# Performance work log

Hardware: AMD Instinct MI355X
Metric: run time of the kernel (lower is better)

Reference implementation:

```python
import jax, jax.numpy as jnp
import numpy as np

N, E, H, IN = 4096, 65536, 256, 16
N_BLOCKS, N_SUB = 3, 2
IE = 2 * H + 2  # edge-mlp input: h[row] ++ h[col] ++ edge_attr(2)
NORM_FACTOR = 100.0


def setup_inputs() -> dict:
    key = jax.random.key(0)
    ks = jax.random.split(key, 24)
    G = N_BLOCKS * N_SUB  # 6 GCLs total

    def p(k, shape, fan_in, gain=1.0):
        return gain * jax.random.normal(k, shape, jnp.float32) / np.sqrt(fan_in)

    return {
        "h": jax.random.normal(ks[0], (N, IN), jnp.float32),
        "x": jax.random.normal(ks[1], (N, 3), jnp.float32),
        "edge_index": jax.random.randint(ks[2], (2, E), 0, N),
        # embedding in/out
        "emb_w": p(ks[3], (IN, H), IN), "emb_b": jnp.zeros((H,), jnp.float32),
        "out_w": p(ks[4], (H, IN), H), "out_b": jnp.zeros((IN,), jnp.float32),
        # GCL edge MLP (stacked over the 6 GCLs)
        "edge_w1": p(ks[5], (G, IE, H), IE), "edge_b1": jnp.zeros((G, H), jnp.float32),
        "edge_w2": p(ks[6], (G, H, H), H), "edge_b2": jnp.zeros((G, H), jnp.float32),
        # GCL node MLP
        "node_w1": p(ks[7], (G, 2 * H, H), 2 * H), "node_b1": jnp.zeros((G, H), jnp.float32),
        "node_w2": p(ks[8], (G, H, H), H), "node_b2": jnp.zeros((G, H), jnp.float32),
        # EquivariantUpdate coord MLP (stacked over 3 blocks); last layer xavier gain=0.001, no bias
        "coord_w1": p(ks[9], (N_BLOCKS, IE, H), IE), "coord_b1": jnp.zeros((N_BLOCKS, H), jnp.float32),
        "coord_w2": p(ks[10], (N_BLOCKS, H, H), H), "coord_b2": jnp.zeros((N_BLOCKS, H), jnp.float32),
        "coord_w3": p(ks[11], (N_BLOCKS, H, 1), H, gain=0.001),
    }


def reference(h, x, edge_index, emb_w, emb_b, out_w, out_b,
              edge_w1, edge_b1, edge_w2, edge_b2,
              node_w1, node_b1, node_w2, node_b2,
              coord_w1, coord_b1, coord_w2, coord_b2, coord_w3):
    row, col = edge_index[0], edge_index[1]
    n_nodes = h.shape[0]

    def seg_sum(data):  # unsorted_segment_sum with 'sum' aggregation / normalization_factor
        return jax.ops.segment_sum(data, row, num_segments=n_nodes) / NORM_FACTOR

    def coord2diff(xc):  # norm_constant = 1
        d = xc[row] - xc[col]                      # [E,3]
        radial = jnp.sum(d * d, axis=1, keepdims=True)  # [E,1]
        cd = d / (jnp.sqrt(radial + 1e-8) + 1.0)
        return radial, cd

    dist0, _ = coord2diff(x)          # EGNN-level distances (from initial coords)
    h = h @ emb_w + emb_b             # node embedding

    gi = 0
    for b in range(N_BLOCKS):
        radial, coord_diff = coord2diff(x)
        ea = jnp.concatenate([radial, dist0], axis=1)   # [E,2] edge_attr
        for _ in range(N_SUB):  # GCL sublayers
            m = jnp.concatenate([h[row], h[col], ea], axis=1)           # [E, 2H+2]
            m = jax.nn.silu(m @ edge_w1[gi] + edge_b1[gi])
            m = jax.nn.silu(m @ edge_w2[gi] + edge_b2[gi])              # [E, H]
            agg = seg_sum(m)                                            # [N, H]
            u = jnp.concatenate([h, agg], axis=1)                       # [N, 2H]
            u = jax.nn.silu(u @ node_w1[gi] + node_b1[gi])
            h = h + u @ node_w2[gi] + node_b2[gi]                       # residual node update
            gi += 1
        # EquivariantUpdate (tanh=False)
        t = jnp.concatenate([h[row], h[col], ea], axis=1)
        t = jax.nn.silu(t @ coord_w1[b] + coord_b1[b])
        t = jax.nn.silu(t @ coord_w2[b] + coord_b2[b])
        trans = coord_diff * (t @ coord_w3[b])                          # [E,3]
        x = x + seg_sum(trans)

    h = h @ out_w + out_b
    return h, x
```

## Files before the change

### kernel.cpp

```cpp
#include <hip/hip_runtime.h>
#include <hip/hip_bf16.h>
#include <cstdint>
#include <cstddef>

#define NN 4096
#define NE 65536
#define HD 256

typedef __attribute__((ext_vector_type(4))) float f32x4;
typedef __attribute__((ext_vector_type(8))) __bf16 bf16x8;

static __device__ __forceinline__ float silu_f(float v) {
  return v / (1.f + __expf(-v));
}

struct TJob { const float* src; __bf16* dst; int K; int N; };
struct TJobs { TJob j[39]; };

__global__ __launch_bounds__(256) void k_transpose(TJobs jobs) {
  TJob jb = jobs.j[blockIdx.z];
  int k0 = blockIdx.x << 5, n0 = blockIdx.y << 5;
  if (k0 >= jb.K || n0 >= jb.N) return;
  __shared__ float t[32][33];
  int tx = threadIdx.x & 31, ty = threadIdx.x >> 5;
#pragma unroll
  for (int r = ty; r < 32; r += 8)
    t[r][tx] = jb.src[(size_t)(k0 + r) * jb.N + n0 + tx];
  __syncthreads();
#pragma unroll
  for (int r = ty; r < 32; r += 8)
    jb.dst[(size_t)(n0 + r) * jb.K + k0 + tx] = (__bf16)t[tx][r];
}

__global__ __launch_bounds__(256) void k_hist(const int* __restrict__ ei, int* __restrict__ cnt) {
  int e = blockIdx.x * 256 + threadIdx.x;
  atomicAdd(&cnt[ei[e]], 1);
}

__global__ __launch_bounds__(1024) void k_scan(const int* __restrict__ cnt, int* __restrict__ offs,
                                               int* __restrict__ cursor) {
  __shared__ int tmp[1024];
  int tid = threadIdx.x;
  int v[4]; int s = 0;
#pragma unroll
  for (int i = 0; i < 4; i++) { v[i] = cnt[tid * 4 + i]; s += v[i]; }
  tmp[tid] = s;
  __syncthreads();
  for (int o = 1; o < 1024; o <<= 1) {
    int t = (tid >= o) ? tmp[tid - o] : 0;
    __syncthreads();
    tmp[tid] += t;
    __syncthreads();
  }
  int base = (tid > 0) ? tmp[tid - 1] : 0;
#pragma unroll
  for (int i = 0; i < 4; i++) {
    offs[tid * 4 + i] = base; cursor[tid * 4 + i] = base; base += v[i];
  }
  if (tid == 1023) offs[4096] = base;
}

__global__ __launch_bounds__(256) void k_scatter(const int* __restrict__ ei, int* __restrict__ cursor,
                                                 int* __restrict__ elist) {
  int e = blockIdx.x * 256 + threadIdx.x;
  int pos = atomicAdd(&cursor[ei[e]], 1);
  elist[pos] = e;
}

__global__ __launch_bounds__(256) void k_csrinit(const int* __restrict__ elist, const int* __restrict__ ei,
                                                 const float* __restrict__ x, int* __restrict__ rowp,
                                                 int* __restrict__ colp, float* __restrict__ d0p) {
  int i = blockIdx.x * 256 + threadIdx.x;
  int e = elist[i];
  int r = ei[e], c = ei[NE + e];
  rowp[i] = r; colp[i] = c;
  float dx = x[r * 3 + 0] - x[c * 3 + 0];
  float dy = x[r * 3 + 1] - x[c * 3 + 1];
  float dz = x[r * 3 + 2] - x[c * 3 + 2];
  d0p[i] = dx * dx + dy * dy + dz * dz;
}

__global__ __launch_bounds__(256) void k_geo(const int* __restrict__ rowp, const int* __restrict__ colp,
                                             const float* __restrict__ x, float* __restrict__ radp,
                                             float* __restrict__ cdp) {
  int i = blockIdx.x * 256 + threadIdx.x;
  int r = rowp[i], c = colp[i];
  float dx = x[r * 3 + 0] - x[c * 3 + 0];
  float dy = x[r * 3 + 1] - x[c * 3 + 1];
  float dz = x[r * 3 + 2] - x[c * 3 + 2];
  float rad = dx * dx + dy * dy + dz * dz;
  radp[i] = rad;
  float inv = 1.f / (sqrtf(rad + 1e-8f) + 1.f);
  cdp[i * 3 + 0] = dx * inv; cdp[i * 3 + 1] = dy * inv; cdp[i * 3 + 2] = dz * inv;
}

__global__ __launch_bounds__(256) void k_copyx(const float* __restrict__ x, float* __restrict__ xc) {
  int i = blockIdx.x * 256 + threadIdx.x;
  if (i < NN * 3) xc[i] = x[i];
}

__global__ __launch_bounds__(256) void k_embed(const float* __restrict__ h0, const float* __restrict__ W,
                                               const float* __restrict__ b, float* __restrict__ hf,
                                               __bf16* __restrict__ h16) {
  int n = blockIdx.x, c = threadIdx.x;
  float s = b[c];
#pragma unroll
  for (int i = 0; i < 16; i++) s += h0[n * 16 + i] * W[i * 256 + c];
  hf[(size_t)n * HD + c] = s;
  h16[(size_t)n * HD + c] = (__bf16)s;
}

__global__ __launch_bounds__(256) void k_segsum(const __bf16* __restrict__ m2p, const int* __restrict__ offs,
                                                const __bf16* __restrict__ h16, __bf16* __restrict__ ncat) {
  __shared__ float sd[8][256];
  int n = blockIdx.x, t = threadIdx.x;
  int g = t >> 5, l = t & 31;
  int c0 = l << 3;
  float a[8] = {};
  int ib = offs[n], ie = offs[n + 1];
  for (int i = ib + g; i < ie; i += 8) {
    bf16x8 v = *(const bf16x8*)(m2p + (size_t)i * 256 + c0);
#pragma unroll
    for (int j = 0; j < 8; j++) a[j] += (float)v[j];
  }
#pragma unroll
  for (int j = 0; j < 8; j++) sd[g][c0 + j] = a[j];
  __syncthreads();
  float s = 0.f;
#pragma unroll
  for (int j = 0; j < 8; j++) s += sd[j][t];
  ncat[(size_t)n * 512 + t] = h16[(size_t)n * HD + t];
  ncat[(size_t)n * 512 + 256 + t] = (__bf16)(s * 0.01f);
}

__global__ __launch_bounds__(256) void k_xupd(const float* __restrict__ transp, const int* __restrict__ offs,
                                              float* __restrict__ xc) {
  int n = blockIdx.x * 256 + threadIdx.x;
  if (n >= NN) return;
  float a0 = 0.f, a1 = 0.f, a2 = 0.f;
  int i1 = offs[n + 1];
  for (int i = offs[n]; i < i1; i++) {
    a0 += transp[i * 3 + 0]; a1 += transp[i * 3 + 1]; a2 += transp[i * 3 + 2];
  }
  xc[n * 3 + 0] += a0 * 0.01f;
  xc[n * 3 + 1] += a1 * 0.01f;
  xc[n * 3 + 2] += a2 * 0.01f;
}

__global__ __launch_bounds__(256) void k_outh(const float* __restrict__ hf, const float* __restrict__ W,
                                              const float* __restrict__ b, float* __restrict__ out) {
  int t = blockIdx.x * 256 + threadIdx.x;
  int n = t >> 4, j = t & 15;
  float s = b[j];
  for (int c = 0; c < 256; c++) s += hf[(size_t)n * HD + c] * W[c * 16 + j];
  out[n * 16 + j] = s;
}

__global__ __launch_bounds__(256) void k_outx(const float* __restrict__ xc, float* __restrict__ out) {
  int i = blockIdx.x * 256 + threadIdx.x;
  if (i < NN * 3) out[i] = xc[i];
}

template <int EPI>
__global__ __launch_bounds__(512, 4) void k_edgeblk(
    const __bf16* __restrict__ PQ, const int* __restrict__ rowp, const int* __restrict__ colp,
    const float* __restrict__ radp, const float* __restrict__ d0p,
    const float* __restrict__ w1r, const float* __restrict__ w1d, const float* __restrict__ b1,
    const __bf16* __restrict__ Bt, const float* __restrict__ b2,
    __bf16* __restrict__ m2p,
    const float* __restrict__ w3, const float* __restrict__ cdp, float* __restrict__ transp) {
  __shared__ alignas(16) char smem[81920];
  __bf16* As = (__bf16*)smem;
  __bf16* Bs = (__bf16*)(smem + 65536);
  float (*reds)[4] = (float(*)[4])smem;

  const int tid = threadIdx.x;
  const int lane = tid & 63;
  const int wave = tid >> 6;
  const int wm = wave >> 2, wn = wave & 3;
  const int m0 = blockIdx.x * 128;

  const int bn = tid >> 1;
  const int bg = (tid & 1) * 2;
  const int bswz0 = (bg ^ ((bn >> 1) & 3)) << 3;
  const int bswz1 = ((bg + 1) ^ ((bn >> 1) & 3)) << 3;

  const int ar = tid >> 2;
  const int aq = tid & 3;
  const int er = rowp[m0 + ar], ec = colp[m0 + ar];
  const float rad = radp[m0 + ar], dd0 = d0p[m0 + ar];

  uint4 br0a = *(const uint4*)(Bt + (size_t)bn * 256 + bg * 8);
  uint4 br0b = *(const uint4*)(Bt + (size_t)bn * 256 + bg * 8 + 8);
  uint4 br1a = *(const uint4*)(Bt + (size_t)bn * 256 + 32 + bg * 8);
  uint4 br1b = *(const uint4*)(Bt + (size_t)bn * 256 + 32 + bg * 8 + 8);
  uint4 breg[2][2];
  breg[0][0] = br0a; breg[0][1] = br0b;
  breg[1][0] = br1a; breg[1][1] = br1b;

#pragma unroll
  for (int i = 0; i < 8; i++) {
    int g = aq + 4 * i;
    int k = g * 8;
    bf16x8 pv = *(const bf16x8*)(PQ + (size_t)er * 512 + k);
    bf16x8 qv = *(const bf16x8*)(PQ + (size_t)ec * 512 + 256 + k);
    float4 wr0 = *(const float4*)(w1r + k),     wr1 = *(const float4*)(w1r + k + 4);
    float4 wd0 = *(const float4*)(w1d + k),     wd1 = *(const float4*)(w1d + k + 4);
    float4 bb0 = *(const float4*)(b1 + k),      bb1 = *(const float4*)(b1 + k + 4);
    bf16x8 o;
    const float* wrp0 = &wr0.x; const float* wdp0 = &wd0.x; const float* bbp0 = &bb0.x;
#pragma unroll
    for (int j = 0; j < 4; j++)
      o[j] = (__bf16)silu_f((float)pv[j] + (float)qv[j] + rad * wrp0[j] + dd0 * wdp0[j] + bbp0[j]);
    const float* wrp1 = &wr1.x; const float* wdp1 = &wd1.x; const float* bbp1 = &bb1.x;
#pragma unroll
    for (int j = 0; j < 4; j++)
      o[4 + j] = (__bf16)silu_f((float)pv[4 + j] + (float)qv[4 + j] + rad * wrp1[j] + dd0 * wdp1[j] + bbp1[j]);
    *(bf16x8*)&As[ar * 256 + ((g ^ (ar & 7)) << 3)] = o;
  }

  *(uint4*)&Bs[bn * 32 + bswz0] = breg[0][0];
  *(uint4*)&Bs[bn * 32 + bswz1] = breg[0][1];
  __syncthreads();

  f32x4 acc[4][4] = {};
  const int kg = lane >> 4;
  const int l15 = lane & 15;

#pragma unroll
  for (int t = 0; t < 8; t++) {
    if (t + 2 < 8) {
      breg[t & 1][0] = *(const uint4*)(Bt + (size_t)bn * 256 + (t + 2) * 32 + bg * 8);
      breg[t & 1][1] = *(const uint4*)(Bt + (size_t)bn * 256 + (t + 2) * 32 + bg * 8 + 8);
    }
    bf16x8 bf[4];
#pragma unroll
    for (int fn = 0; fn < 4; fn++) {
      int n = wn * 64 + fn * 16 + l15;
      bf[fn] = *(const bf16x8*)&Bs[n * 32 + ((kg ^ ((n >> 1) & 3)) << 3)];
    }
#pragma unroll
    for (int fm = 0; fm < 4; fm++) {
      int r = wm * 64 + fm * 16 + l15;
      int G = t * 4 + kg;
      bf16x8 af = *(const bf16x8*)&As[r * 256 + ((G ^ (r & 7)) << 3)];
#pragma unroll
      for (int fn = 0; fn < 4; fn++)
        acc[fm][fn] = __builtin_amdgcn_mfma_f32_16x16x32_bf16(af, bf[fn], acc[fm][fn], 0, 0, 0);
    }
    __syncthreads();
    if (t < 7) {
      *(uint4*)&Bs[bn * 32 + bswz0] = breg[(t + 1) & 1][0];
      *(uint4*)&Bs[bn * 32 + bswz1] = breg[(t + 1) & 1][1];
      __syncthreads();
    }
  }

  if (EPI == 0) {
#pragma unroll
    for (int fm = 0; fm < 4; fm++) {
#pragma unroll
      for (int j = 0; j < 4; j++) {
        size_t row = m0 + wm * 64 + fm * 16 + ((lane >> 4) << 2) + j;
#pragma unroll
        for (int fn = 0; fn < 4; fn++) {
          int col = wn * 64 + fn * 16 + l15;
          m2p[row * 256 + col] = (__bf16)silu_f(acc[fm][fn][j] + b2[col]);
        }
      }
    }
  } else {
    float s[4][4];
#pragma unroll
    for (int fm = 0; fm < 4; fm++)
#pragma unroll
      for (int j = 0; j < 4; j++) s[fm][j] = 0.f;
#pragma unroll
    for (int fn = 0; fn < 4; fn++) {
      int col = wn * 64 + fn * 16 + l15;
      float bv = b2[col], wv = w3[col];
#pragma unroll
      for (int fm = 0; fm < 4; fm++)
#pragma unroll
        for (int j = 0; j < 4; j++)
          s[fm][j] += silu_f(acc[fm][fn][j] + bv) * wv;
    }
#pragma unroll
    for (int off = 1; off < 16; off <<= 1)
#pragma unroll
      for (int fm = 0; fm < 4; fm++)
#pragma unroll
        for (int j = 0; j < 4; j++)
          s[fm][j] += __shfl_xor(s[fm][j], off, 64);
    if (l15 == 0) {
#pragma unroll
      for (int fm = 0; fm < 4; fm++)
#pragma unroll
        for (int j = 0; j < 4; j++)
          reds[wm * 64 + fm * 16 + ((lane >> 4) << 2) + j][wn] = s[fm][j];
    }
    __syncthreads();
    if (tid < 128) {
      float sv = reds[tid][0] + reds[tid][1] + reds[tid][2] + reds[tid][3];
      size_t i = (size_t)m0 + tid;
      transp[i * 3 + 0] = cdp[i * 3 + 0] * sv;
      transp[i * 3 + 1] = cdp[i * 3 + 1] * sv;
      transp[i * 3 + 2] = cdp[i * 3 + 2] * sv;
    }
  }
}

template <int EPI>
__global__ __launch_bounds__(256) void k_gemm64(const __bf16* __restrict__ A, const __bf16* __restrict__ Bt,
                                                const float* __restrict__ bias, __bf16* __restrict__ outb,
                                                float* __restrict__ outf, int M, int N, int K) {
  constexpr int BM = 64, BN = 64, BK = 64;
  __shared__ __bf16 As[2][BM * BK];
  __shared__ __bf16 Bs[2][BN * BK];
  const int tid = threadIdx.x;
  const int lane = tid & 63;
  const int wave = tid >> 6;
  const int wm = wave >> 1, wn = wave & 1;
  const size_t m0 = (size_t)blockIdx.x * BM;
  const size_t n0 = (size_t)blockIdx.y * BN;
  const int r0 = tid >> 3, g0 = tid & 7;
  const int gs0 = (g0 ^ (r0 & 7)) << 3;

  f32x4 acc[2][2] = {};
  const int NT = K >> 6;

  {
    uint4 a0 = *(const uint4*)(A + (m0 + r0) * K + g0 * 8);
    uint4 a1 = *(const uint4*)(A + (m0 + r0 + 32) * K + g0 * 8);
    uint4 b0 = *(const uint4*)(Bt + (n0 + r0) * K + g0 * 8);
    uint4 b1 = *(const uint4*)(Bt + (n0 + r0 + 32) * K + g0 * 8);
    *(uint4*)&As[0][r0 * BK + gs0] = a0;
    *(uint4*)&As[0][(r0 + 32) * BK + gs0] = a1;
    *(uint4*)&Bs[0][r0 * BK + gs0] = b0;
    *(uint4*)&Bs[0][(r0 + 32) * BK + gs0] = b1;
  }
  __syncthreads();

  int buf = 0;
  for (int t = 0; t < NT; ++t) {
    const bool has = (t + 1 < NT);
    uint4 a0, a1, b0, b1;
    if (has) {
      int kt = (t + 1) << 6;
      a0 = *(const uint4*)(A + (m0 + r0) * K + kt + g0 * 8);
      a1 = *(const uint4*)(A + (m0 + r0 + 32) * K + kt + g0 * 8);
      b0 = *(const uint4*)(Bt + (n0 + r0) * K + kt + g0 * 8);
      b1 = *(const uint4*)(Bt + (n0 + r0 + 32) * K + kt + g0 * 8);
    }
#pragma unroll
    for (int ks = 0; ks < BK; ks += 32) {
      const int kg = (ks >> 3) + (lane >> 4);
      bf16x8 af[2], bfv[2];
#pragma unroll
      for (int fm = 0; fm < 2; fm++) {
        int r = wm * 32 + fm * 16 + (lane & 15);
        af[fm] = *(const bf16x8*)&As[buf][r * BK + ((kg ^ (r & 7)) << 3)];
      }
#pragma unroll
      for (int fn = 0; fn < 2; fn++) {
        int r = wn * 32 + fn * 16 + (lane & 15);
        bfv[fn] = *(const bf16x8*)&Bs[buf][r * BK + ((kg ^ (r & 7)) << 3)];
      }
#pragma unroll
      for (int fm = 0; fm < 2; fm++)
#pragma unroll
        for (int fn = 0; fn < 2; fn++)
          acc[fm][fn] = __builtin_amdgcn_mfma_f32_16x16x32_bf16(af[fm], bfv[fn], acc[fm][fn], 0, 0, 0);
    }
    if (has) {
      *(uint4*)&As[buf ^ 1][r0 * BK + gs0] = a0;
      *(uint4*)&As[buf ^ 1][(r0 + 32) * BK + gs0] = a1;
      *(uint4*)&Bs[buf ^ 1][r0 * BK + gs0] = b0;
      *(uint4*)&Bs[buf ^ 1][(r0 + 32) * BK + gs0] = b1;
    }
    __syncthreads();
    buf ^= 1;
  }

#pragma unroll
  for (int fm = 0; fm < 2; fm++) {
#pragma unroll
    for (int fn = 0; fn < 2; fn++) {
      const size_t col = n0 + wn * 32 + fn * 16 + (lane & 15);
      float bv = (EPI == 4) ? 0.f : bias[col];
#pragma unroll
      for (int j = 0; j < 4; j++) {
        size_t row = m0 + wm * 32 + fm * 16 + ((lane >> 4) << 2) + j;
        size_t idx = row * (size_t)N + col;
        float v = acc[fm][fn][j] + bv;
        if (EPI == 1) {
          outb[idx] = (__bf16)silu_f(v);
        } else if (EPI == 2) {
          float nh = outf[idx] + v;
          outf[idx] = nh;
          outb[idx] = (__bf16)nh;
        } else {
          outb[idx] = (__bf16)v;
        }
      }
    }
  }
}

extern "C" void kernel_launch(void* const* d_in, const int* in_sizes, int n_in,
                              void* d_out, int out_size, void* d_ws, size_t ws_size,
                              hipStream_t stream) {
  const float* h_in    = (const float*)d_in[0];
  const float* x_in    = (const float*)d_in[1];
  const int*   ei      = (const int*)d_in[2];
  const float* emb_w   = (const float*)d_in[3];
  const float* emb_b   = (const float*)d_in[4];
  const float* out_w   = (const float*)d_in[5];
  const float* out_b   = (const float*)d_in[6];
  const float* edge_w1 = (const float*)d_in[7];
  const float* edge_b1 = (const float*)d_in[8];
  const float* edge_w2 = (const float*)d_in[9];
  const float* edge_b2 = (const float*)d_in[10];
  const float* node_w1 = (const float*)d_in[11];
  const float* node_b1 = (const float*)d_in[12];
  const float* node_w2 = (const float*)d_in[13];
  const float* node_b2 = (const float*)d_in[14];
  const float* coord_w1 = (const float*)d_in[15];
  const float* coord_b1 = (const float*)d_in[16];
  const float* coord_w2 = (const float*)d_in[17];
  const float* coord_b2 = (const float*)d_in[18];
  const float* coord_w3 = (const float*)d_in[19];

  char* p = (char*)d_ws;
  auto alloc = [&](size_t bytes) -> void* {
    void* r = (void*)p;
    p += (bytes + 255) & ~(size_t)255;
    return r;
  };
  __bf16* e1T  = (__bf16*)alloc((size_t)6 * 512 * 256 * 2);
  __bf16* e2T  = (__bf16*)alloc((size_t)6 * 256 * 256 * 2);
  __bf16* n1T  = (__bf16*)alloc((size_t)6 * 256 * 512 * 2);
  __bf16* n2T  = (__bf16*)alloc((size_t)6 * 256 * 256 * 2);
  __bf16* c1T  = (__bf16*)alloc((size_t)3 * 512 * 256 * 2);
  __bf16* c2T  = (__bf16*)alloc((size_t)3 * 256 * 256 * 2);
  __bf16* h16  = (__bf16*)alloc((size_t)NN * HD * 2);
  __bf16* PQ16 = (__bf16*)alloc((size_t)NN * 512 * 2);
  __bf16* m2p  = (__bf16*)alloc((size_t)NE * HD * 2);
  __bf16* ncat = (__bf16*)alloc((size_t)NN * 512 * 2);
  __bf16* u    = (__bf16*)alloc((size_t)NN * HD * 2);
  float* hf    = (float*)alloc((size_t)NN * HD * 4);
  float* xc    = (float*)alloc((size_t)NN * 3 * 4);
  float* d0p   = (float*)alloc((size_t)NE * 4);
  float* radp  = (float*)alloc((size_t)NE * 4);
  float* cdp   = (float*)alloc((size_t)NE * 3 * 4);
  float* transp = (float*)alloc((size_t)NE * 3 * 4);
  int* cnt     = (int*)alloc((size_t)NN * 4);
  int* offs    = (int*)alloc((size_t)(NN + 1) * 4);
  int* cursor  = (int*)alloc((size_t)NN * 4);
  int* elist   = (int*)alloc((size_t)NE * 4);
  int* rowp    = (int*)alloc((size_t)NE * 4);
  int* colp    = (int*)alloc((size_t)NE * 4);

  TJobs jobs;
  int nj = 0;
  for (int gi = 0; gi < 6; gi++) {
    jobs.j[nj++] = { edge_w1 + (size_t)gi * 514 * 256,             e1T + (size_t)gi * 512 * 256,             256, 256 };
    jobs.j[nj++] = { edge_w1 + (size_t)gi * 514 * 256 + 256 * 256, e1T + (size_t)gi * 512 * 256 + 256 * 256, 256, 256 };
    jobs.j[nj++] = { edge_w2 + (size_t)gi * 256 * 256,             e2T + (size_t)gi * 256 * 256,             256, 256 };
    jobs.j[nj++] = { node_w1 + (size_t)gi * 512 * 256,             n1T + (size_t)gi * 256 * 512,             512, 256 };
    jobs.j[nj++] = { node_w2 + (size_t)gi * 256 * 256,             n2T + (size_t)gi * 256 * 256,             256, 256 };
  }
  for (int b = 0; b < 3; b++) {
    jobs.j[nj++] = { coord_w1 + (size_t)b * 514 * 256,             c1T + (size_t)b * 512 * 256,              256, 256 };
    jobs.j[nj++] = { coord_w1 + (size_t)b * 514 * 256 + 256 * 256, c1T + (size_t)b * 512 * 256 + 256 * 256,  256, 256 };
    jobs.j[nj++] = { coord_w2 + (size_t)b * 256 * 256,             c2T + (size_t)b * 256 * 256,              256, 256 };
  }

  hipMemsetAsync(cnt, 0, (size_t)NN * 4, stream);
  k_transpose<<<dim3(16, 8, 39), 256, 0, stream>>>(jobs);
  k_hist<<<NE / 256, 256, 0, stream>>>(ei, cnt);
  k_scan<<<1, 1024, 0, stream>>>(cnt, offs, cursor);
  k_scatter<<<NE / 256, 256, 0, stream>>>(ei, cursor, elist);
  k_csrinit<<<NE / 256, 256, 0, stream>>>(elist, ei, x_in, rowp, colp, d0p);
  k_copyx<<<(NN * 3 + 255) / 256, 256, 0, stream>>>(x_in, xc);
  k_embed<<<NN, 256, 0, stream>>>(h_in, emb_w, emb_b, hf, h16);

  int gi = 0;
  for (int b = 0; b < 3; b++) {
    k_geo<<<NE / 256, 256, 0, stream>>>(rowp, colp, xc, radp, cdp);
    for (int s = 0; s < 2; s++, gi++) {
      const float* w1 = edge_w1 + (size_t)gi * 514 * 256;
      k_gemm64<4><<<dim3(64, 8), 256, 0, stream>>>(
          h16, e1T + (size_t)gi * 512 * 256, nullptr, PQ16, nullptr, NN, 512, 256);
      k_edgeblk<0><<<NE / 128, 512, 0, stream>>>(
          PQ16, rowp, colp, radp, d0p, w1 + 512 * 256, w1 + 513 * 256, edge_b1 + gi * 256,
          e2T + (size_t)gi * 256 * 256, edge_b2 + gi * 256, m2p, nullptr, nullptr, nullptr);
      k_segsum<<<NN, 256, 0, stream>>>(m2p, offs, h16, ncat);
      k_gemm64<1><<<dim3(64, 4), 256, 0, stream>>>(
          ncat, n1T + (size_t)gi * 256 * 512, node_b1 + gi * 256, u, nullptr, NN, 256, 512);
      k_gemm64<2><<<dim3(64, 4), 256, 0, stream>>>(
          u, n2T + (size_t)gi * 256 * 256, node_b2 + gi * 256, h16, hf, NN, 256, 256);
    }
    const float* w1c = coord_w1 + (size_t)b * 514 * 256;
    k_gemm64<4><<<dim3(64, 8), 256, 0, stream>>>(
        h16, c1T + (size_t)b * 512 * 256, nullptr, PQ16, nullptr, NN, 512, 256);
    k_edgeblk<1><<<NE / 128, 512, 0, stream>>>(
        PQ16, rowp, colp, radp, d0p, w1c + 512 * 256, w1c + 513 * 256, coord_b1 + b * 256,
        c2T + (size_t)b * 256 * 256, coord_b2 + b * 256, nullptr,
        coord_w3 + (size_t)b * 256, cdp, transp);
    k_xupd<<<NN / 256, 256, 0, stream>>>(transp, offs, xc);
  }
  k_outh<<<NN * 16 / 256, 256, 0, stream>>>(hf, out_w, out_b, (float*)d_out);
  k_outx<<<(NN * 3 + 255) / 256, 256, 0, stream>>>(xc, (float*)d_out + (size_t)NN * 16);
}
```

Baseline: 516.3 us.

## Double-buffer edge GEMM B tiles, read split node-MLP input, merge small kernels

The edge block kernel now uses two shared-memory B buffers, which drops one barrier per K step. Its LDS grows to 96KB and the launch bound falls to 2 blocks per SM. The node MLP GEMM reads h16 and the aggregate from two separate buffers, so segsum no longer copies h into a concatenated buffer. The x copy is folded into csrinit and the two output kernels are merged into one, cutting launch count. The lower occupancy bound may hurt latency hiding.

Result: slower. 804.3 us (+55.8%).

```diff
diff --git a/kernel.cpp b/kernel.cpp
--- a/kernel.cpp
+++ b/kernel.cpp
@@ -69,8 +69,10 @@
 
 __global__ __launch_bounds__(256) void k_csrinit(const int* __restrict__ elist, const int* __restrict__ ei,
                                                  const float* __restrict__ x, int* __restrict__ rowp,
-                                                 int* __restrict__ colp, float* __restrict__ d0p) {
+                                                 int* __restrict__ colp, float* __restrict__ d0p,
+                                                 float* __restrict__ xc) {
   int i = blockIdx.x * 256 + threadIdx.x;
+  if (i < NN * 3) xc[i] = x[i];
   int e = elist[i];
   int r = ei[e], c = ei[NE + e];
   rowp[i] = r; colp[i] = c;
@@ -94,11 +96,6 @@
   cdp[i * 3 + 0] = dx * inv; cdp[i * 3 + 1] = dy * inv; cdp[i * 3 + 2] = dz * inv;
 }
 
-__global__ __launch_bounds__(256) void k_copyx(const float* __restrict__ x, float* __restrict__ xc) {
-  int i = blockIdx.x * 256 + threadIdx.x;
-  if (i < NN * 3) xc[i] = x[i];
-}
-
 __global__ __launch_bounds__(256) void k_embed(const float* __restrict__ h0, const float* __restrict__ W,
                                                const float* __restrict__ b, float* __restrict__ hf,
                                                __bf16* __restrict__ h16) {
@@ -111,7 +108,7 @@
 }
 
 __global__ __launch_bounds__(256) void k_segsum(const __bf16* __restrict__ m2p, const int* __restrict__ offs,
-                                                const __bf16* __restrict__ h16, __bf16* __restrict__ ncat) {
+                                                __bf16* __restrict__ agg16) {
   __shared__ float sd[8][256];
   int n = blockIdx.x, t = threadIdx.x;
   int g = t >> 5, l = t & 31;
@@ -129,8 +126,7 @@
   float s = 0.f;
 #pragma unroll
   for (int j = 0; j < 8; j++) s += sd[j][t];
-  ncat[(size_t)n * 512 + t] = h16[(size_t)n * HD + t];
-  ncat[(size_t)n * 512 + 256 + t] = (__bf16)(s * 0.01f);
+  agg16[(size_t)n * 256 + t] = (__bf16)(s * 0.01f);
 }
 
 __global__ __launch_bounds__(256) void k_xupd(const float* __restrict__ transp, const int* __restrict__ offs,
@@ -147,31 +143,33 @@
   xc[n * 3 + 2] += a2 * 0.01f;
 }
 
-__global__ __launch_bounds__(256) void k_outh(const float* __restrict__ hf, const float* __restrict__ W,
-                                              const float* __restrict__ b, float* __restrict__ out) {
+__global__ __launch_bounds__(256) void k_out(const float* __restrict__ hf, const float* __restrict__ W,
+                                             const float* __restrict__ b, const float* __restrict__ xc,
+                                             float* __restrict__ out) {
   int t = blockIdx.x * 256 + threadIdx.x;
-  int n = t >> 4, j = t & 15;
-  float s = b[j];
-  for (int c = 0; c < 256; c++) s += hf[(size_t)n * HD + c] * W[c * 16 + j];
-  out[n * 16 + j] = s;
-}
-
-__global__ __launch_bounds__(256) void k_outx(const float* __restrict__ xc, float* __restrict__ out) {
-  int i = blockIdx.x * 256 + threadIdx.x;
-  if (i < NN * 3) out[i] = xc[i];
+  if (blockIdx.x < 256) {
+    int n = t >> 4, j = t & 15;
+    float s = b[j];
+    for (int c = 0; c < 256; c++) s += hf[(size_t)n * HD + c] * W[c * 16 + j];
+    out[n * 16 + j] = s;
+  } else {
+    int i = t - NN * 16;
+    if (i < NN * 3) out[NN * 16 + i] = xc[i];
+  }
 }
 
 template <int EPI>
-__global__ __launch_bounds__(512, 4) void k_edgeblk(
+__global__ __launch_bounds__(512, 2) void k_edgeblk(
     const __bf16* __restrict__ PQ, const int* __restrict__ rowp, const int* __restrict__ colp,
     const float* __restrict__ radp, const float* __restrict__ d0p,
     const float* __restrict__ w1r, const float* __restrict__ w1d, const float* __restrict__ b1,
     const __bf16* __restrict__ Bt, const float* __restrict__ b2,
     __bf16* __restrict__ m2p,
     const float* __restrict__ w3, const float* __restrict__ cdp, float* __restrict__ transp) {
-  __shared__ alignas(16) char smem[81920];
-  __bf16* As = (__bf16*)smem;
-  __bf16* Bs = (__bf16*)(smem + 65536);
+  __shared__ alignas(16) char smem[98304];
+  __bf16* As  = (__bf16*)smem;
+  __bf16* BsA = (__bf16*)(smem + 65536);
+  __bf16* BsB = (__bf16*)(smem + 81920);
   float (*reds)[4] = (float(*)[4])smem;
 
   const int tid = threadIdx.x;
@@ -179,65 +177,61 @@
   const int wave = tid >> 6;
   const int wm = wave >> 2, wn = wave & 3;
   const int m0 = blockIdx.x * 128;
-
-  const int bn = tid >> 1;
-  const int bg = (tid & 1) * 2;
-  const int bswz0 = (bg ^ ((bn >> 1) & 3)) << 3;
-  const int bswz1 = ((bg + 1) ^ ((bn >> 1) & 3)) << 3;
-
-  const int ar = tid >> 2;
-  const int aq = tid & 3;
-  const int er = rowp[m0 + ar], ec = colp[m0 + ar];
-  const float rad = radp[m0 + ar], dd0 = d0p[m0 + ar];
-
-  uint4 br0a = *(const uint4*)(Bt + (size_t)bn * 256 + bg * 8);
-  uint4 br0b = *(const uint4*)(Bt + (size_t)bn * 256 + bg * 8 + 8);
-  uint4 br1a = *(const uint4*)(Bt + (size_t)bn * 256 + 32 + bg * 8);
-  uint4 br1b = *(const uint4*)(Bt + (size_t)bn * 256 + 32 + bg * 8 + 8);
-  uint4 breg[2][2];
-  breg[0][0] = br0a; breg[0][1] = br0b;
-  breg[1][0] = br1a; breg[1][1] = br1b;
-
-#pragma unroll
-  for (int i = 0; i < 8; i++) {
-    int g = aq + 4 * i;
-    int k = g * 8;
-    bf16x8 pv = *(const bf16x8*)(PQ + (size_t)er * 512 + k);
-    bf16x8 qv = *(const bf16x8*)(PQ + (size_t)ec * 512 + 256 + k);
-    float4 wr0 = *(const float4*)(w1r + k),     wr1 = *(const float4*)(w1r + k + 4);
-    float4 wd0 = *(const float4*)(w1d + k),     wd1 = *(const float4*)(w1d + k + 4);
-    float4 bb0 = *(const float4*)(b1 + k),      bb1 = *(const float4*)(b1 + k + 4);
-    bf16x8 o;
-    const float* wrp0 = &wr0.x; const float* wdp0 = &wd0.x; const float* bbp0 = &bb0.x;
-#pragma unroll
-    for (int j = 0; j < 4; j++)
-      o[j] = (__bf16)silu_f((float)pv[j] + (float)qv[j] + rad * wrp0[j] + dd0 * wdp0[j] + bbp0[j]);
-    const float* wrp1 = &wr1.x; const float* wdp1 = &wd1.x; const float* bbp1 = &bb1.x;
-#pragma unroll
-    for (int j = 0; j < 4; j++)
-      o[4 + j] = (__bf16)silu_f((float)pv[4 + j] + (float)qv[4 + j] + rad * wrp1[j] + dd0 * wdp1[j] + bbp1[j]);
-    *(bf16x8*)&As[ar * 256 + ((g ^ (ar & 7)) << 3)] = o;
-  }
-
-  *(uint4*)&Bs[bn * 32 + bswz0] = breg[0][0];
-  *(uint4*)&Bs[bn * 32 + bswz1] = breg[0][1];
+  const int l15 = lane & 15, kg = lane >> 4;
+
+  const int bn = tid >> 1, bg = (tid & 1) * 2;
+  const int bo0 = (bg ^ ((bn >> 1) & 3)) << 3;
+  const int bo1 = ((bg + 1) ^ ((bn >> 1) & 3)) << 3;
+
+  uint4 rb[2][2];
+  rb[0][0] = *(const uint4*)(Bt + (size_t)bn * 256 + bg * 8);
+  rb[0][1] = *(const uint4*)(Bt + (size_t)bn * 256 + (bg + 1) * 8);
+  rb[1][0] = *(const uint4*)(Bt + (size_t)bn * 256 + 32 + bg * 8);
+  rb[1][1] = *(const uint4*)(Bt + (size_t)bn * 256 + 32 + (bg + 1) * 8);
+
+  {
+    const int ar = tid >> 2, aq = tid & 3;
+    const int er = rowp[m0 + ar], ec = colp[m0 + ar];
+    const float rad = radp[m0 + ar], dd0 = d0p[m0 + ar];
+#pragma unroll
+    for (int i = 0; i < 8; i++) {
+      int g = aq + 4 * i;
+      int k = g * 8;
+      bf16x8 pv = *(const bf16x8*)(PQ + (size_t)er * 512 + k);
+      bf16x8 qv = *(const bf16x8*)(PQ + (size_t)ec * 512 + 256 + k);
+      float4 wr0 = *(const float4*)(w1r + k), wr1 = *(const float4*)(w1r + k + 4);
+      float4 wd0 = *(const float4*)(w1d + k), wd1 = *(const float4*)(w1d + k + 4);
+      float4 bb0 = *(const float4*)(b1 + k),  bb1 = *(const float4*)(b1 + k + 4);
+      bf16x8 o;
+      const float* wrp0 = &wr0.x; const float* wdp0 = &wd0.x; const float* bbp0 = &bb0.x;
+#pragma unroll
+      for (int j = 0; j < 4; j++)
+        o[j] = (__bf16)silu_f((float)pv[j] + (float)qv[j] + rad * wrp0[j] + dd0 * wdp0[j] + bbp0[j]);
+      const float* wrp1 = &wr1.x; const float* wdp1 = &wd1.x; const float* bbp1 = &bb1.x;
+#pragma unroll
+      for (int j = 0; j < 4; j++)
+        o[4 + j] = (__bf16)silu_f((float)pv[4 + j] + (float)qv[4 + j] + rad * wrp1[j] + dd0 * wdp1[j] + bbp1[j]);
+      *(bf16x8*)&As[ar * 256 + ((g ^ (ar & 7)) << 3)] = o;
+    }
+  }
+
+  *(uint4*)&BsA[bn * 32 + bo0] = rb[0][0];
+  *(uint4*)&BsA[bn * 32 + bo1] = rb[0][1];
   __syncthreads();
 
   f32x4 acc[4][4] = {};
-  const int kg = lane >> 4;
-  const int l15 = lane & 15;
-
 #pragma unroll
   for (int t = 0; t < 8; t++) {
     if (t + 2 < 8) {
-      breg[t & 1][0] = *(const uint4*)(Bt + (size_t)bn * 256 + (t + 2) * 32 + bg * 8);
-      breg[t & 1][1] = *(const uint4*)(Bt + (size_t)bn * 256 + (t + 2) * 32 + bg * 8 + 8);
-    }
+      rb[t & 1][0] = *(const uint4*)(Bt + (size_t)bn * 256 + (t + 2) * 32 + bg * 8);
+      rb[t & 1][1] = *(const uint4*)(Bt + (size_t)bn * 256 + (t + 2) * 32 + (bg + 1) * 8);
+    }
+    const __bf16* Bsc = (t & 1) ? BsB : BsA;
     bf16x8 bf[4];
 #pragma unroll
     for (int fn = 0; fn < 4; fn++) {
       int n = wn * 64 + fn * 16 + l15;
-      bf[fn] = *(const bf16x8*)&Bs[n * 32 + ((kg ^ ((n >> 1) & 3)) << 3)];
+      bf[fn] = *(const bf16x8*)&Bsc[n * 32 + ((kg ^ ((n >> 1) & 3)) << 3)];
     }
 #pragma unroll
     for (int fm = 0; fm < 4; fm++) {
@@ -248,10 +242,10 @@
       for (int fn = 0; fn < 4; fn++)
         acc[fm][fn] = __builtin_amdgcn_mfma_f32_16x16x32_bf16(af, bf[fn], acc[fm][fn], 0, 0, 0);
     }
-    __syncthreads();
-    if (t < 7) {
-      *(uint4*)&Bs[bn * 32 + bswz0] = breg[(t + 1) & 1][0];
-      *(uint4*)&Bs[bn * 32 + bswz1] = breg[(t + 1) & 1][1];
+    if (t + 1 < 8) {
+      __bf16* Bsn = (t & 1) ? BsA : BsB;
+      *(uint4*)&Bsn[bn * 32 + bo0] = rb[(t + 1) & 1][0];
+      *(uint4*)&Bsn[bn * 32 + bo1] = rb[(t + 1) & 1][1];
       __syncthreads();
     }
   }
@@ -292,6 +286,7 @@
 #pragma unroll
         for (int j = 0; j < 4; j++)
           s[fm][j] += __shfl_xor(s[fm][j], off, 64);
+    __syncthreads();
     if (l15 == 0) {
 #pragma unroll
       for (int fm = 0; fm < 4; fm++)
@@ -310,8 +305,9 @@
   }
 }
 
-template <int EPI>
-__global__ __launch_bounds__(256) void k_gemm64(const __bf16* __restrict__ A, const __bf16* __restrict__ Bt,
+template <int EPI, int SPLIT>
+__global__ __launch_bounds__(256) void k_gemm64(const __bf16* __restrict__ A, const __bf16* __restrict__ A2,
+                                                const __bf16* __restrict__ Bt,
                                                 const float* __restrict__ bias, __bf16* __restrict__ outb,
                                                 float* __restrict__ outf, int M, int N, int K) {
   constexpr int BM = 64, BN = 64, BK = 64;
@@ -325,13 +321,14 @@
   const size_t n0 = (size_t)blockIdx.y * BN;
   const int r0 = tid >> 3, g0 = tid & 7;
   const int gs0 = (g0 ^ (r0 & 7)) << 3;
+  const int Astride = SPLIT ? 256 : K;
 
   f32x4 acc[2][2] = {};
   const int NT = K >> 6;
 
   {
-    uint4 a0 = *(const uint4*)(A + (m0 + r0) * K + g0 * 8);
-    uint4 a1 = *(const uint4*)(A + (m0 + r0 + 32) * K + g0 * 8);
+    uint4 a0 = *(const uint4*)(A + (m0 + r0) * Astride + g0 * 8);
+    uint4 a1 = *(const uint4*)(A + (m0 + r0 + 32) * Astride + g0 * 8);
     uint4 b0 = *(const uint4*)(Bt + (n0 + r0) * K + g0 * 8);
     uint4 b1 = *(const uint4*)(Bt + (n0 + r0 + 32) * K + g0 * 8);
     *(uint4*)&As[0][r0 * BK + gs0] = a0;
@@ -347,8 +344,12 @@
     uint4 a0, a1, b0, b1;
     if (has) {
       int kt = (t + 1) << 6;
-      a0 = *(const uint4*)(A + (m0 + r0) * K + kt + g0 * 8);
-      a1 = *(const uint4*)(A + (m0 + r0 + 32) * K + kt + g0 * 8);
+      const __bf16* Ab;
+      int ko;
+      if (SPLIT) { Ab = (kt < 256) ? A : A2; ko = kt & 255; }
+      else       { Ab = A; ko = kt; }
+      a0 = *(const uint4*)(Ab + (m0 + r0) * Astride + ko + g0 * 8);
+      a1 = *(const uint4*)(Ab + (m0 + r0 + 32) * Astride + ko + g0 * 8);
       b0 = *(const uint4*)(Bt + (n0 + r0) * K + kt + g0 * 8);
       b1 = *(const uint4*)(Bt + (n0 + r0 + 32) * K + kt + g0 * 8);
     }
@@ -446,7 +447,7 @@
   __bf16* h16  = (__bf16*)alloc((size_t)NN * HD * 2);
   __bf16* PQ16 = (__bf16*)alloc((size_t)NN * 512 * 2);
   __bf16* m2p  = (__bf16*)alloc((size_t)NE * HD * 2);
-  __bf16* ncat = (__bf16*)alloc((size_t)NN * 512 * 2);
+  __bf16* agg16 = (__bf16*)alloc((size_t)NN * HD * 2);
   __bf16* u    = (__bf16*)alloc((size_t)NN * HD * 2);
   float* hf    = (float*)alloc((size_t)NN * HD * 4);
   float* xc    = (float*)alloc((size_t)NN * 3 * 4);
@@ -481,8 +482,7 @@
   k_hist<<<NE / 256, 256, 0, stream>>>(ei, cnt);
   k_scan<<<1, 1024, 0, stream>>>(cnt, offs, cursor);
   k_scatter<<<NE / 256, 256, 0, stream>>>(ei, cursor, elist);
-  k_csrinit<<<NE / 256, 256, 0, stream>>>(elist, ei, x_in, rowp, colp, d0p);
-  k_copyx<<<(NN * 3 + 255) / 256, 256, 0, stream>>>(x_in, xc);
+  k_csrinit<<<NE / 256, 256, 0, stream>>>(elist, ei, x_in, rowp, colp, d0p, xc);
   k_embed<<<NN, 256, 0, stream>>>(h_in, emb_w, emb_b, hf, h16);
 
   int gi = 0;
@@ -490,26 +490,25 @@
     k_geo<<<NE / 256, 256, 0, stream>>>(rowp, colp, xc, radp, cdp);
     for (int s = 0; s < 2; s++, gi++) {
       const float* w1 = edge_w1 + (size_t)gi * 514 * 256;
-      k_gemm64<4><<<dim3(64, 8), 256, 0, stream>>>(
-          h16, e1T + (size_t)gi * 512 * 256, nullptr, PQ16, nullptr, NN, 512, 256);
+      k_gemm64<4, 0><<<dim3(64, 8), 256, 0, stream>>>(
+          h16, nullptr, e1T + (size_t)gi * 512 * 256, nullptr, PQ16, nullptr, NN, 512, 256);
       k_edgeblk<0><<<NE / 128, 512, 0, stream>>>(
           PQ16, rowp, colp, radp, d0p, w1 + 512 * 256, w1 + 513 * 256, edge_b1 + gi * 256,
           e2T + (size_t)gi * 256 * 256, edge_b2 + gi * 256, m2p, nullptr, nullptr, nullptr);
-      k_segsum<<<NN, 256, 0, stream>>>(m2p, offs, h16, ncat);
-      k_gemm64<1><<<dim3(64, 4), 256, 0, stream>>>(
-          ncat, n1T + (size_t)gi * 256 * 512, node_b1 + gi * 256, u, nullptr, NN, 256, 512);
-      k_gemm64<2><<<dim3(64, 4), 256, 0, stream>>>(
-          u, n2T + (size_t)gi * 256 * 256, node_b2 + gi * 256, h16, hf, NN, 256, 256);
+      k_segsum<<<NN, 256, 0, stream>>>(m2p, offs, agg16);
+      k_gemm64<1, 1><<<dim3(64, 4), 256, 0, stream>>>(
+          h16, agg16, n1T + (size_t)gi * 256 * 512, node_b1 + gi * 256, u, nullptr, NN, 256, 512);
+      k_gemm64<2, 0><<<dim3(64, 4), 256, 0, stream>>>(
+          u, nullptr, n2T + (size_t)gi * 256 * 256, node_b2 + gi * 256, h16, hf, NN, 256, 256);
     }
     const float* w1c = coord_w1 + (size_t)b * 514 * 256;
-    k_gemm64<4><<<dim3(64, 8), 256, 0, stream>>>(
-        h16, c1T + (size_t)b * 512 * 256, nullptr, PQ16, nullptr, NN, 512, 256);
+    k_gemm64<4, 0><<<dim3(64, 8), 256, 0, stream>>>(
+        h16, nullptr, c1T + (size_t)b * 512 * 256, nullptr, PQ16, nullptr, NN, 512, 256);
     k_edgeblk<1><<<NE / 128, 512, 0, stream>>>(
         PQ16, rowp, colp, radp, d0p, w1c + 512 * 256, w1c + 513 * 256, coord_b1 + b * 256,
         c2T + (size_t)b * 256 * 256, coord_b2 + b * 256, nullptr,
         coord_w3 + (size_t)b * 256, cdp, transp);
     k_xupd<<<NN / 256, 256, 0, stream>>>(transp, offs, xc);
   }
-  k_outh<<<NN * 16 / 256, 256, 0, stream>>>(hf, out_w, out_b, (float*)d_out);
-  k_outx<<<(NN * 3 + 255) / 256, 256, 0, stream>>>(xc, (float*)d_out + (size_t)NN * 16);
-}
+  k_out<<<256 + 48, 256, 0, stream>>>(hf, out_w, out_b, xc, (float*)d_out);
+}
```
